# Performance work log

Measured on AMD Instinct MI355X. Metric: run time of the kernel, lower is better.

## Reference

```python
import jax, jax.numpy as jnp
import numpy as np

N_HEAD = 16
N_KV_HEAD = 4
D_MODEL = 2048
D_HEAD = 128
D_OUT = 2048
N_REP = N_HEAD // N_KV_HEAD
Q_INNER = N_HEAD * D_HEAD
KV_INNER = N_KV_HEAD * D_HEAD
B, S = 2, 2048


def setup_inputs() -> dict:
    key = jax.random.key(0)
    ks = jax.random.split(key, 10)
    sc = lambda fan_in: 1.0 / np.sqrt(fan_in)
    return {
        "hidden_state": jax.random.normal(ks[0], (B, S, D_MODEL), dtype=jnp.float32),
        "attention_mask": jnp.ones((B, 1, S, S), dtype=jnp.int32),
        "Wq": jax.random.uniform(ks[1], (Q_INNER, D_MODEL), jnp.float32, -sc(D_MODEL), sc(D_MODEL)),
        "bq": jax.random.uniform(ks[2], (Q_INNER,), jnp.float32, -sc(D_MODEL), sc(D_MODEL)),
        "Wk": jax.random.uniform(ks[3], (KV_INNER, D_MODEL), jnp.float32, -sc(D_MODEL), sc(D_MODEL)),
        "bk": jax.random.uniform(ks[4], (KV_INNER,), jnp.float32, -sc(D_MODEL), sc(D_MODEL)),
        "Wv": jax.random.uniform(ks[5], (KV_INNER, D_MODEL), jnp.float32, -sc(D_MODEL), sc(D_MODEL)),
        "bv": jax.random.uniform(ks[6], (KV_INNER,), jnp.float32, -sc(D_MODEL), sc(D_MODEL)),
        "Wo": jax.random.uniform(ks[7], (D_OUT, Q_INNER), jnp.float32, -sc(Q_INNER), sc(Q_INNER)),
        "bo": jax.random.uniform(ks[8], (D_OUT,), jnp.float32, -sc(Q_INNER), sc(Q_INNER)),
    }


def reference(hidden_state, attention_mask, Wq, bq, Wk, bk, Wv, bv, Wo, bo):
    b, s, _ = hidden_state.shape
    # projections (torch Linear: x @ W.T + b)
    q = hidden_state @ Wq.T + bq                    # [b, s, n_head*d_head]
    k = hidden_state @ Wk.T + bk                    # [b, s, n_kv*d_head]
    v = hidden_state @ Wv.T + bv
    q = q.reshape(b, s, N_HEAD, D_HEAD).transpose(0, 2, 1, 3)      # [b, h, s, d]
    k = k.reshape(b, s, N_KV_HEAD, D_HEAD).transpose(0, 2, 1, 3)   # [b, kh, s, d]
    v = v.reshape(b, s, N_KV_HEAD, D_HEAD).transpose(0, 2, 1, 3)
    # repeat_kv: expand kv heads to n_head
    k = jnp.repeat(k, N_REP, axis=1)                # [b, h, s, d]
    v = jnp.repeat(v, N_REP, axis=1)
    scores = jnp.einsum("bhqd,bhkd->bhqk", q, k) / jnp.sqrt(jnp.float32(D_HEAD))
    scores = jnp.where(attention_mask == 0, -jnp.inf, scores)
    probs = jax.nn.softmax(scores, axis=-1)         # [b, h, s, s]
    out = jnp.einsum("bhqk,bhkd->bhqd", probs, v)   # [b, h, s, d]
    out = out.transpose(0, 2, 1, 3).reshape(b, s, Q_INNER)
    return out @ Wo.T + bo                          # [b, s, d_out]
```

## Files before the change

### kernel.cpp

```cpp
#include <hip/hip_runtime.h>

typedef unsigned short u16;
typedef unsigned int u32;
typedef __attribute__((ext_vector_type(4))) float f32x4;
typedef __attribute__((ext_vector_type(16))) float f32x16;
typedef __attribute__((ext_vector_type(2))) u32 u32x2;
typedef __attribute__((ext_vector_type(4))) u32 u32x4;
typedef __attribute__((ext_vector_type(8))) __bf16 bf16x8;

#define QSCALE (0.08838834764831845f * 1.44269504088896340736f)

__device__ __forceinline__ u16 f2bf(float x) {
  u32 u = __builtin_bit_cast(u32, x);
  u32 r = (u + 0x7FFFu + ((u >> 16) & 1u)) >> 16;
  return (u16)r;
}

__device__ __forceinline__ u16 cvt_bf16(float x) {
  __bf16 b = (__bf16)x;
  return __builtin_bit_cast(u16, b);
}

__device__ __forceinline__ u32 pk2(float lo, float hi) {
  return (u32)cvt_bf16(lo) | ((u32)cvt_bf16(hi) << 16);
}

__device__ __forceinline__ f32x16 mfma32(bf16x8 a, bf16x8 b, f32x16 c) {
  return __builtin_amdgcn_mfma_f32_32x32x16_bf16(a, b, c, 0, 0, 0);
}

#define GLDS16(g, l)                                              \
  __builtin_amdgcn_global_load_lds(                               \
      (const __attribute__((address_space(1))) void*)(g),         \
      (__attribute__((address_space(3))) void*)(l), 16, 0, 0)

__global__ __launch_bounds__(256) void cvt5_kernel(
    const float* __restrict__ s0, const float* __restrict__ s1,
    const float* __restrict__ s2, const float* __restrict__ s3,
    const float* __restrict__ s4, u16* __restrict__ d0, u16* __restrict__ d1,
    u16* __restrict__ d2, u16* __restrict__ d3, u16* __restrict__ d4) {
  const int bid = blockIdx.x;
  const float* s;
  u16* d;
  int base;
  if (bid < 4096) { s = s0; d = d0; base = 0; }
  else if (bid < 6144) { s = s1; d = d1; base = 4096; }
  else if (bid < 6656) { s = s2; d = d2; base = 6144; }
  else if (bid < 7168) { s = s3; d = d3; base = 6656; }
  else { s = s4; d = d4; base = 7168; }
  size_t i = (size_t)(bid - base) * 256 + threadIdx.x;
  float4 a = ((const float4*)s)[2 * i];
  float4 b = ((const float4*)s)[2 * i + 1];
  uint4 r;
  r.x = f2bf(a.x) | ((u32)f2bf(a.y) << 16);
  r.y = f2bf(a.z) | ((u32)f2bf(a.w) << 16);
  r.z = f2bf(b.x) | ((u32)f2bf(b.y) << 16);
  r.w = f2bf(b.z) | ((u32)f2bf(b.w) << 16);
  ((uint4*)d)[i] = r;
}

__device__ __forceinline__ void gemm_bt_core(const u16* __restrict__ A,
                                             const u16* __restrict__ B, int K,
                                             int bm, int bn, u16* As, u16* Bs,
                                             f32x4 acc[4][4]) {
  const int tid = threadIdx.x;
  const int lane = tid & 63;
  const int w = tid >> 6;
  const int wm = (w >> 1) * 64;
  const int wn = (w & 1) * 64;
  const int r0 = lane & 15;
  const int g = lane >> 4;

  for (int k0 = 0; k0 < K; k0 += 64) {
#pragma unroll
    for (int i = 0; i < 4; ++i) {
      const int gi = i * 256 + tid;
      const int row = gi >> 3, gc = gi & 7;
      const int scol = (gc ^ (row & 7)) * 8;
      GLDS16(A + (size_t)(bm + row) * K + k0 + scol, As + gi * 8);
      GLDS16(B + (size_t)(bn + row) * K + k0 + scol, Bs + gi * 8);
    }
    __syncthreads();
#pragma unroll
    for (int kh = 0; kh < 2; ++kh) {
      bf16x8 af[4], bf[4];
#pragma unroll
      for (int mi = 0; mi < 4; ++mi) {
        const int row = wm + mi * 16 + r0;
        af[mi] = *(const bf16x8*)&As[row * 64 + (((kh * 4 + g) ^ (row & 7)) * 8)];
      }
#pragma unroll
      for (int ni = 0; ni < 4; ++ni) {
        const int row = wn + ni * 16 + r0;
        bf[ni] = *(const bf16x8*)&Bs[row * 64 + (((kh * 4 + g) ^ (row & 7)) * 8)];
      }
#pragma unroll
      for (int mi = 0; mi < 4; ++mi)
#pragma unroll
        for (int ni = 0; ni < 4; ++ni)
          acc[mi][ni] = __builtin_amdgcn_mfma_f32_16x16x32_bf16(
              af[mi], bf[ni], acc[mi][ni], 0, 0, 0);
    }
    __syncthreads();
  }
}

__global__ __launch_bounds__(256, 3) void qkv_gemm(
    const u16* __restrict__ A, const u16* __restrict__ B,
    const float* __restrict__ bq, const float* __restrict__ bk,
    const float* __restrict__ bv, u16* __restrict__ qb, u16* __restrict__ kb,
    u16* __restrict__ vtb) {
  __shared__ u16 As[8192], Bs[8192];
  f32x4 acc[4][4];
#pragma unroll
  for (int i = 0; i < 4; ++i)
#pragma unroll
    for (int j = 0; j < 4; ++j) acc[i][j] = f32x4{0.f, 0.f, 0.f, 0.f};
  const int bm = blockIdx.y * 128, bn = blockIdx.x * 128;
  gemm_bt_core(A, B, 2048, bm, bn, As, Bs, acc);
  const int lane = threadIdx.x & 63, w = threadIdx.x >> 6;
  const int wm = (w >> 1) * 64, wn = (w & 1) * 64;
  const int r0 = lane & 15, g = lane >> 4;
#pragma unroll
  for (int ni = 0; ni < 4; ++ni) {
    const int n = bn + wn + ni * 16 + r0;
#pragma unroll
    for (int mi = 0; mi < 4; ++mi) {
      f32x4 v = acc[mi][ni];
#pragma unroll
      for (int r = 0; r < 4; ++r) {
        const int m = bm + wm + mi * 16 + g * 4 + r;
        const int b = m >> 11, s = m & 2047;
        const float val = v[r];
        if (n < 2048) {
          const int h = n >> 7, d = n & 127;
          qb[((size_t)(b * 16 + h) * 2048 + s) * 128 + d] =
              f2bf((val + bq[n]) * QSCALE);
        } else if (n < 2560) {
          const int nn = n - 2048, kh = nn >> 7, d = nn & 127;
          kb[((size_t)(b * 4 + kh) * 2048 + s) * 128 + d] = f2bf(val + bk[nn]);
        } else {
          const int nn = n - 2560, kh = nn >> 7, d = nn & 127;
          vtb[((size_t)(b * 4 + kh) * 128 + d) * 2048 + s] = f2bf(val + bv[nn]);
        }
      }
    }
  }
}

__global__ __launch_bounds__(256, 3) void oproj_gemm(const u16* __restrict__ A,
                                                     const u16* __restrict__ B,
                                                     const float* __restrict__ bo,
                                                     float* __restrict__ out) {
  __shared__ u16 As[8192], Bs[8192];
  f32x4 acc[4][4];
#pragma unroll
  for (int i = 0; i < 4; ++i)
#pragma unroll
    for (int j = 0; j < 4; ++j) acc[i][j] = f32x4{0.f, 0.f, 0.f, 0.f};
  const int bm = blockIdx.y * 128, bn = blockIdx.x * 128;
  gemm_bt_core(A, B, 2048, bm, bn, As, Bs, acc);
  const int lane = threadIdx.x & 63, w = threadIdx.x >> 6;
  const int wm = (w >> 1) * 64, wn = (w & 1) * 64;
  const int r0 = lane & 15, g = lane >> 4;
#pragma unroll
  for (int ni = 0; ni < 4; ++ni) {
    const int n = bn + wn + ni * 16 + r0;
    const float bb = bo[n];
#pragma unroll
    for (int mi = 0; mi < 4; ++mi) {
#pragma unroll
      for (int r = 0; r < 4; ++r) {
        const int m = bm + wm + mi * 16 + g * 4 + r;
        out[(size_t)m * 2048 + n] = acc[mi][ni][r] + bb;
      }
    }
  }
}

__global__ __launch_bounds__(256, 2) void attn_kernel(const u16* __restrict__ q,
                                                      const u16* __restrict__ k,
                                                      const u16* __restrict__ vt,
                                                      u16* __restrict__ o) {
  __shared__ u16 Ks[2][8192];
  __shared__ u16 Vs[2][8192];
  const int tid = threadIdx.x, lane = tid & 63, w = tid >> 6;
  const int l31 = lane & 31, hi = lane >> 5;
  const int id = blockIdx.x;
  const int xcd = id & 7;
  const int b = xcd >> 2, kh = xcd & 3;
  const int j = id >> 3;
  const int h = kh * 4 + (j & 3);
  const int qt = j >> 2;
  const int q0 = qt * 128 + w * 32;
  const u16* qh = q + ((size_t)(b * 16 + h) * 2048 + q0) * 128;
  const u16* kp = k + (size_t)(b * 4 + kh) * 2048 * 128;
  const u16* vp = vt + (size_t)(b * 4 + kh) * 128 * 2048;

  bf16x8 qa[8];
#pragma unroll
  for (int dc = 0; dc < 8; ++dc)
    qa[dc] = *(const bf16x8*)&qh[(size_t)l31 * 128 + dc * 16 + hi * 8];

  f32x16 oacc[4];
#pragma unroll
  for (int dt = 0; dt < 4; ++dt) oacc[dt] = (f32x16)(0.f);
  f32x16 lacc = (f32x16)(0.f);
  float mrun = -INFINITY;

  u32x4 onev;
  onev[0] = onev[1] = onev[2] = onev[3] = 0x3F803F80u;
  const bf16x8 ones_b = __builtin_bit_cast(bf16x8, onev);

  const int gB = w * 64 + lane;

#define STAGE_KV(cur, t)                                                       \
  do {                                                                         \
    const u16* kt_ = kp + (size_t)(t) * 64 * 128;                              \
    _Pragma("unroll") for (int i_ = 0; i_ < 4; ++i_) {                         \
      int gi_ = i_ * 256 + gB;                                                 \
      int row_ = gi_ >> 4, gc_ = gi_ & 15;                                     \
      GLDS16(kt_ + row_ * 128 + ((gc_ ^ (row_ & 15)) * 8),                     \
             &Ks[cur][(i_ * 256 + w * 64) * 8]);                               \
    }                                                                          \
    _Pragma("unroll") for (int i_ = 0; i_ < 4; ++i_) {                         \
      int gi_ = i_ * 256 + gB;                                                 \
      int row_ = gi_ >> 3, gc_ = gi_ & 7;                                      \
      GLDS16(vp + (size_t)row_ * 2048 + (t) * 64 + ((gc_ ^ (row_ & 7)) * 8),   \
             &Vs[cur][(i_ * 256 + w * 64) * 8]);                               \
    }                                                                          \
  } while (0)

  STAGE_KV(0, 0);
  __syncthreads();
  int cur = 0;

  for (int t = 0; t < 32; ++t) {
    if (t < 31) STAGE_KV(cur ^ 1, t + 1);

    f32x16 s0v = (f32x16)(0.f), s1v = (f32x16)(0.f);
    __builtin_amdgcn_s_setprio(1);
#pragma unroll
    for (int dc = 0; dc < 8; ++dc) {
      const int gc = dc * 2 + hi;
      const int ro0 = l31, ro1 = 32 + l31;
      bf16x8 kf0 = *(const bf16x8*)&Ks[cur][ro0 * 128 + ((gc ^ (ro0 & 15)) << 3)];
      bf16x8 kf1 = *(const bf16x8*)&Ks[cur][ro1 * 128 + ((gc ^ (ro1 & 15)) << 3)];
      s0v = mfma32(kf0, qa[dc], s0v);
      s1v = mfma32(kf1, qa[dc], s1v);
    }
    __builtin_amdgcn_s_setprio(0);

    float m8[8];
#pragma unroll
    for (int i = 0; i < 8; ++i)
      m8[i] = fmaxf(fmaxf(s0v[i], s0v[i + 8]), fmaxf(s1v[i], s1v[i + 8]));
    float mx = fmaxf(fmaxf(fmaxf(m8[0], m8[1]), fmaxf(m8[2], m8[3])),
                     fmaxf(fmaxf(m8[4], m8[5]), fmaxf(m8[6], m8[7])));
    mx = fmaxf(mx, __shfl_xor(mx, 32));
    if (__any(mx > mrun + 8.f)) {
      const float mnew = fmaxf(mrun, mx);
      const float alpha = __builtin_amdgcn_exp2f(mrun - mnew);
      mrun = mnew;
#pragma unroll
      for (int r = 0; r < 16; ++r) {
        const float ar = __shfl(alpha, ((r & 3) + 8 * (r >> 2)) + (hi << 2));
        lacc[r] *= ar;
#pragma unroll
        for (int dt = 0; dt < 4; ++dt) oacc[dt][r] *= ar;
      }
    }
#pragma unroll
    for (int i = 0; i < 16; ++i) {
      s0v[i] = __builtin_amdgcn_exp2f(s0v[i] - mrun);
      s1v[i] = __builtin_amdgcn_exp2f(s1v[i] - mrun);
    }

    __builtin_amdgcn_s_setprio(1);
#pragma unroll
    for (int c = 0; c < 4; ++c) {
      const float* sv = (c < 2) ? (const float*)&s0v : (const float*)&s1v;
      const int base = (c & 1) * 8;
      u32x4 fw;
      fw[0] = pk2(sv[base + 0], sv[base + 1]);
      fw[1] = pk2(sv[base + 2], sv[base + 3]);
      fw[2] = pk2(sv[base + 4], sv[base + 5]);
      fw[3] = pk2(sv[base + 6], sv[base + 7]);
      const bf16x8 pf = __builtin_bit_cast(bf16x8, fw);
      lacc = mfma32(pf, ones_b, lacc);
#pragma unroll
      for (int dt = 0; dt < 4; ++dt) {
        const int d = dt * 32 + l31;
        const u32x2 vlo =
            *(const u32x2*)&Vs[cur][d * 64 + (((2 * c) ^ (d & 7)) << 3) + 4 * hi];
        const u32x2 vhi =
            *(const u32x2*)&Vs[cur][d * 64 + (((2 * c + 1) ^ (d & 7)) << 3) + 4 * hi];
        u32x4 vv;
        vv[0] = vlo[0]; vv[1] = vlo[1]; vv[2] = vhi[0]; vv[3] = vhi[1];
        oacc[dt] = mfma32(pf, __builtin_bit_cast(bf16x8, vv), oacc[dt]);
      }
    }
    __builtin_amdgcn_s_setprio(0);

    __syncthreads();
    cur ^= 1;
  }
#undef STAGE_KV

#pragma unroll
  for (int r = 0; r < 16; ++r) {
    const float linv = 1.f / lacc[r];
    const int row = q0 + (r & 3) + 8 * (r >> 2) + (hi << 2);
#pragma unroll
    for (int dt = 0; dt < 4; ++dt)
      o[(size_t)(b * 2048 + row) * 2048 + h * 128 + dt * 32 + l31] =
          cvt_bf16(oacc[dt][r] * linv);
  }
}

extern "C" void kernel_launch(void* const* d_in, const int* in_sizes, int n_in,
                              void* d_out, int out_size, void* d_ws,
                              size_t ws_size, hipStream_t stream) {
  (void)in_sizes; (void)n_in; (void)out_size; (void)ws_size;
  const float* hidden = (const float*)d_in[0];
  const float* Wq = (const float*)d_in[2];
  const float* bq = (const float*)d_in[3];
  const float* Wk = (const float*)d_in[4];
  const float* bk = (const float*)d_in[5];
  const float* Wv = (const float*)d_in[6];
  const float* bv = (const float*)d_in[7];
  const float* Wo = (const float*)d_in[8];
  const float* bo = (const float*)d_in[9];
  float* out = (float*)d_out;
  char* ws = (char*)d_ws;

  u16* hidb = (u16*)(ws + 0);
  u16* wcat = (u16*)(ws + 16777216);
  u16* wob  = (u16*)(ws + 29360128);
  u16* qb   = (u16*)(ws + 37748736);
  u16* kb   = (u16*)(ws + 54525952);
  u16* vtb  = (u16*)(ws + 58720256);
  u16* attb = (u16*)(ws + 62914560);

  cvt5_kernel<<<9216, 256, 0, stream>>>(hidden, Wq, Wk, Wv, Wo, hidb, wcat,
                                        wcat + (size_t)2048 * 2048,
                                        wcat + (size_t)2560 * 2048, wob);

  qkv_gemm<<<dim3(24, 32), 256, 0, stream>>>(hidb, wcat, bq, bk, bv, qb, kb, vtb);
  attn_kernel<<<512, 256, 0, stream>>>(qb, kb, vtb, attb);
  oproj_gemm<<<dim3(16, 32), 256, 0, stream>>>(attb, wob, bo, out);
}
```

Baseline: 208.0 us.

## Software-pipeline QK^T one tile ahead with triple-buffered K in attention

Restructures the attention inner loop so the QK^T MFMAs for tile t+1 are issued alongside the softmax and PV work of tile t. K is now triple-buffered and prefetched two tiles ahead, while V stays double-buffered. The loop is fully unrolled with alternating score registers. The goal is to hide the exp/max softmax latency behind matrix work, at the cost of more LDS (one extra 16KB K buffer), more live registers and larger code, which may hurt occupancy at launch_bounds(256,2).

```diff
diff --git a/kernel.cpp b/kernel.cpp
--- a/kernel.cpp
+++ b/kernel.cpp
@@ -182,7 +182,7 @@
                                                       const u16* __restrict__ k,
                                                       const u16* __restrict__ vt,
                                                       u16* __restrict__ o) {
-  __shared__ u16 Ks[2][8192];
+  __shared__ u16 Ks[3][8192];
   __shared__ u16 Vs[2][8192];
   const int tid = threadIdx.x, lane = tid & 63, w = tid >> 6;
   const int l31 = lane & 31, hi = lane >> 5;
@@ -214,98 +214,116 @@
 
   const int gB = w * 64 + lane;
 
-#define STAGE_KV(cur, t)                                                       \
+#define STAGE_K(buf, t)                                                        \
   do {                                                                         \
     const u16* kt_ = kp + (size_t)(t) * 64 * 128;                              \
     _Pragma("unroll") for (int i_ = 0; i_ < 4; ++i_) {                         \
       int gi_ = i_ * 256 + gB;                                                 \
       int row_ = gi_ >> 4, gc_ = gi_ & 15;                                     \
       GLDS16(kt_ + row_ * 128 + ((gc_ ^ (row_ & 15)) * 8),                     \
-             &Ks[cur][(i_ * 256 + w * 64) * 8]);                               \
-    }                                                                          \
+             &Ks[buf][(i_ * 256 + w * 64) * 8]);                               \
+    }                                                                          \
+  } while (0)
+
+#define STAGE_V(buf, t)                                                        \
+  do {                                                                         \
     _Pragma("unroll") for (int i_ = 0; i_ < 4; ++i_) {                         \
       int gi_ = i_ * 256 + gB;                                                 \
       int row_ = gi_ >> 3, gc_ = gi_ & 7;                                      \
       GLDS16(vp + (size_t)row_ * 2048 + (t) * 64 + ((gc_ ^ (row_ & 7)) * 8),   \
-             &Vs[cur][(i_ * 256 + w * 64) * 8]);                               \
+             &Vs[buf][(i_ * 256 + w * 64) * 8]);                               \
     }                                                                          \
   } while (0)
 
-  STAGE_KV(0, 0);
+#define QK_TILE(kb, d0, d1)                                                    \
+  do {                                                                         \
+    _Pragma("unroll") for (int dc = 0; dc < 8; ++dc) {                         \
+      const int gc = dc * 2 + hi;                                              \
+      const int ro0 = l31, ro1 = 32 + l31;                                     \
+      bf16x8 kf0 = *(const bf16x8*)&Ks[kb][ro0 * 128 + ((gc ^ (ro0 & 15)) << 3)]; \
+      bf16x8 kf1 = *(const bf16x8*)&Ks[kb][ro1 * 128 + ((gc ^ (ro1 & 15)) << 3)]; \
+      d0 = mfma32(kf0, qa[dc], d0);                                            \
+      d1 = mfma32(kf1, qa[dc], d1);                                            \
+    }                                                                          \
+  } while (0)
+
+#define BODY(T, sc0, sc1, sn0, sn1)                                            \
+  {                                                                            \
+    const int t_ = (T);                                                        \
+    if (t_ < 30) STAGE_K((t_ + 2) % 3, t_ + 2);                                \
+    if (t_ < 31) STAGE_V((t_ + 1) & 1, t_ + 1);                                \
+    sn0 = (f32x16)(0.f);                                                       \
+    sn1 = (f32x16)(0.f);                                                       \
+    __builtin_amdgcn_s_setprio(1);                                             \
+    if (t_ < 31) {                                                             \
+      const int kb_ = (t_ + 1) % 3;                                            \
+      QK_TILE(kb_, sn0, sn1);           \
+    }                                                                          \
+    __builtin_amdgcn_s_setprio(0);                                             \
+                \
+    float m8[8];                                                               \
+    _Pragma("unroll") for (int i = 0; i < 8; ++i)                              \
+        m8[i] = fmaxf(fmaxf(sc0[i], sc0[i + 8]), fmaxf(sc1[i], sc1[i + 8]));   \
+    float mx = fmaxf(fmaxf(fmaxf(m8[0], m8[1]), fmaxf(m8[2], m8[3])),          \
+                     fmaxf(fmaxf(m8[4], m8[5]), fmaxf(m8[6], m8[7])));         \
+    mx = fmaxf(mx, __shfl_xor(mx, 32));                                        \
+    if (__any(mx > mrun + 8.f)) {                                              \
+      const float mnew = fmaxf(mrun, mx);                                      \
+      const float alpha = __builtin_amdgcn_exp2f(mrun - mnew);                 \
+      mrun = mnew;                                                             \
+      _Pragma("unroll") for (int r = 0; r < 16; ++r) {                         \
+        const float ar = __shfl(alpha, ((r & 3) + 8 * (r >> 2)) + (hi << 2));  \
+        lacc[r] *= ar;                                                         \
+        _Pragma("unroll") for (int dt = 0; dt < 4; ++dt) oacc[dt][r] *= ar;    \
+      }                                                                        \
+    }                                                                          \
+    _Pragma("unroll") for (int i = 0; i < 16; ++i) {                           \
+      sc0[i] = __builtin_amdgcn_exp2f(sc0[i] - mrun);                          \
+      sc1[i] = __builtin_amdgcn_exp2f(sc1[i] - mrun);                          \
+    }                                                                          \
+      \
+    __builtin_amdgcn_s_setprio(1);                                             \
+    _Pragma("unroll") for (int c = 0; c < 4; ++c) {                            \
+      const float* sv = (c < 2) ? (const float*)&sc0 : (const float*)&sc1;     \
+      const int base = (c & 1) * 8;                                            \
+      u32x4 fw;                                                                \
+      fw[0] = pk2(sv[base + 0], sv[base + 1]);                                 \
+      fw[1] = pk2(sv[base + 2], sv[base + 3]);                                 \
+      fw[2] = pk2(sv[base + 4], sv[base + 5]);                                 \
+      fw[3] = pk2(sv[base + 6], sv[base + 7]);                                 \
+      const bf16x8 pf = __builtin_bit_cast(bf16x8, fw);                        \
+      lacc = mfma32(pf, ones_b, lacc);                                         \
+      _Pragma("unroll") for (int dt = 0; dt < 4; ++dt) {                       \
+        const int d = dt * 32 + l31;                                           \
+        const u32x2 vlo = *(const u32x2*)&Vs[t_ & 1]                           \
+            [d * 64 + (((2 * c) ^ (d & 7)) << 3) + 4 * hi];                    \
+        const u32x2 vhi = *(const u32x2*)&Vs[t_ & 1]                           \
+            [d * 64 + (((2 * c + 1) ^ (d & 7)) << 3) + 4 * hi];                \
+        u32x4 vv;                                                              \
+        vv[0] = vlo[0]; vv[1] = vlo[1]; vv[2] = vhi[0]; vv[3] = vhi[1];        \
+        oacc[dt] = mfma32(pf, __builtin_bit_cast(bf16x8, vv), oacc[dt]);       \
+      }                                                                        \
+    }                                                                          \
+    __builtin_amdgcn_s_setprio(0);                                             \
+    if (t_ < 31) __syncthreads();                                              \
+  }
+
+  STAGE_K(0, 0);
+  STAGE_K(1, 1);
+  STAGE_V(0, 0);
   __syncthreads();
-  int cur = 0;
-
-  for (int t = 0; t < 32; ++t) {
-    if (t < 31) STAGE_KV(cur ^ 1, t + 1);
-
-    f32x16 s0v = (f32x16)(0.f), s1v = (f32x16)(0.f);
-    __builtin_amdgcn_s_setprio(1);
-#pragma unroll
-    for (int dc = 0; dc < 8; ++dc) {
-      const int gc = dc * 2 + hi;
-      const int ro0 = l31, ro1 = 32 + l31;
-      bf16x8 kf0 = *(const bf16x8*)&Ks[cur][ro0 * 128 + ((gc ^ (ro0 & 15)) << 3)];
-      bf16x8 kf1 = *(const bf16x8*)&Ks[cur][ro1 * 128 + ((gc ^ (ro1 & 15)) << 3)];
-      s0v = mfma32(kf0, qa[dc], s0v);
-      s1v = mfma32(kf1, qa[dc], s1v);
-    }
-    __builtin_amdgcn_s_setprio(0);
-
-    float m8[8];
-#pragma unroll
-    for (int i = 0; i < 8; ++i)
-      m8[i] = fmaxf(fmaxf(s0v[i], s0v[i + 8]), fmaxf(s1v[i], s1v[i + 8]));
-    float mx = fmaxf(fmaxf(fmaxf(m8[0], m8[1]), fmaxf(m8[2], m8[3])),
-                     fmaxf(fmaxf(m8[4], m8[5]), fmaxf(m8[6], m8[7])));
-    mx = fmaxf(mx, __shfl_xor(mx, 32));
-    if (__any(mx > mrun + 8.f)) {
-      const float mnew = fmaxf(mrun, mx);
-      const float alpha = __builtin_amdgcn_exp2f(mrun - mnew);
-      mrun = mnew;
-#pragma unroll
-      for (int r = 0; r < 16; ++r) {
-        const float ar = __shfl(alpha, ((r & 3) + 8 * (r >> 2)) + (hi << 2));
-        lacc[r] *= ar;
-#pragma unroll
-        for (int dt = 0; dt < 4; ++dt) oacc[dt][r] *= ar;
-      }
-    }
-#pragma unroll
-    for (int i = 0; i < 16; ++i) {
-      s0v[i] = __builtin_amdgcn_exp2f(s0v[i] - mrun);
-      s1v[i] = __builtin_amdgcn_exp2f(s1v[i] - mrun);
-    }
-
-    __builtin_amdgcn_s_setprio(1);
-#pragma unroll
-    for (int c = 0; c < 4; ++c) {
-      const float* sv = (c < 2) ? (const float*)&s0v : (const float*)&s1v;
-      const int base = (c & 1) * 8;
-      u32x4 fw;
-      fw[0] = pk2(sv[base + 0], sv[base + 1]);
-      fw[1] = pk2(sv[base + 2], sv[base + 3]);
-      fw[2] = pk2(sv[base + 4], sv[base + 5]);
-      fw[3] = pk2(sv[base + 6], sv[base + 7]);
-      const bf16x8 pf = __builtin_bit_cast(bf16x8, fw);
-      lacc = mfma32(pf, ones_b, lacc);
-#pragma unroll
-      for (int dt = 0; dt < 4; ++dt) {
-        const int d = dt * 32 + l31;
-        const u32x2 vlo =
-            *(const u32x2*)&Vs[cur][d * 64 + (((2 * c) ^ (d & 7)) << 3) + 4 * hi];
-        const u32x2 vhi =
-            *(const u32x2*)&Vs[cur][d * 64 + (((2 * c + 1) ^ (d & 7)) << 3) + 4 * hi];
-        u32x4 vv;
-        vv[0] = vlo[0]; vv[1] = vlo[1]; vv[2] = vhi[0]; vv[3] = vhi[1];
-        oacc[dt] = mfma32(pf, __builtin_bit_cast(bf16x8, vv), oacc[dt]);
-      }
-    }
-    __builtin_amdgcn_s_setprio(0);
-
-    __syncthreads();
-    cur ^= 1;
-  }
-#undef STAGE_KV
+  f32x16 sA0 = (f32x16)(0.f), sA1 = (f32x16)(0.f), sB0, sB1;
+  QK_TILE(0, sA0, sA1);
+
+#pragma unroll
+  for (int tt = 0; tt < 16; ++tt) {
+    BODY(2 * tt, sA0, sA1, sB0, sB1);
+    BODY(2 * tt + 1, sB0, sB1, sA0, sA1);
+  }
+#undef BODY
+#undef QK_TILE
+#undef STAGE_K
+#undef STAGE_V
 
 #pragma unroll
   for (int r = 0; r < 16; ++r) {
```

Measured after the change: 205.4 us. Within noise of the previous version (-1.2%).
